# Performance work log

Hardware: AMD Instinct MI355X
Metric: run time of the kernel (lower is better)

## Reference

```python
import jax, jax.numpy as jnp
import numpy as np

EPS = 1e-7
TRUNC = 0.5          # truncation level of the robust L1 objective
K_CAND = 64          # max number of piecewise-linear extrema evaluated per row


def _pad_inf(v):
    # (B, n) -> (B, n+2) with -inf / +inf sentinels (torch _pad_inf)
    b = v.shape[0]
    return jnp.concatenate(
        [jnp.full((b, 1), -jnp.inf, v.dtype), v, jnp.full((b, 1), jnp.inf, v.dtype)], axis=-1)


def _pad_cumsum(c):
    # (B, n) -> (B, n+2): leading zero, trailing repeat of last (torch _pad_cumsum)
    return jnp.concatenate([jnp.zeros_like(c[:, :1]), c, c[:, -1:]], axis=-1)


_search_l = jax.vmap(lambda a, v: jnp.searchsorted(a, v, side='left'))
_search_r = jax.vmap(lambda a, v: jnp.searchsorted(a, v, side='right'))


def _align_trunc(x, y, w):
    # Solves min_a sum_i min(TRUNC, w_i * |a*x_i - y_i|) per row. x,y,w: (B, n).
    sign = jnp.sign(x)
    x = x * sign
    y = y * sign
    wx = w * x
    wy = w * y
    ydx = y / jnp.maximum(x, EPS)                       # breakpoints of |a x - y|
    cand_b = (wy - TRUNC) / jnp.maximum(wx, EPS)        # breakpoints where residual hits trunc
    cand_c = (wy + TRUNC) / jnp.maximum(wx, EPS)

    def sorted_cum(v):
        order = jnp.argsort(v, axis=-1)
        vs = jnp.take_along_axis(v, order, axis=-1)
        q = jnp.cumsum(jnp.take_along_axis(wx, order, axis=-1), axis=-1)
        return _pad_inf(vs), _pad_cumsum(q)

    As, QA = sorted_cum(ydx)
    Bs, QB = sorted_cum(cand_b)
    Cs, QC = sorted_cum(cand_c)

    def deriv(search):
        jA = search(As, ydx) - 1
        jB = search(Bs, ydx) - 1
        jC = search(Cs, ydx) - 1
        return (2 * jnp.take_along_axis(QA, jA, axis=-1)
                - jnp.take_along_axis(QB, jB, axis=-1)
                - jnp.take_along_axis(QC, jC, axis=-1))

    left_d = deriv(_search_l)
    right_d = deriv(_search_r)
    is_ext = (left_d < 0) & (right_d >= 0)
    is_ext = is_ext.at[:, 0].set(is_ext[:, 0] | ~jnp.any(is_ext, axis=-1))

    # first K_CAND extrema indices per row (stable sort: extrema=False-key first)
    cand_idx = jnp.argsort(~is_ext, axis=-1, stable=True)[:, :K_CAND]   # (B, K)
    valid = jnp.take_along_axis(is_ext, cand_idx, axis=-1)
    cand_a = jnp.take_along_axis(ydx, cand_idx, axis=-1)                # (B, K)

    # truncated-L1 residual at each candidate a: (B, K)
    res = jnp.sum(
        jnp.minimum(jnp.abs(cand_a[:, :, None] * x[:, None, :] - y[:, None, :]) * w[:, None, :], TRUNC),
        axis=-1)
    res = jnp.where(valid, res, jnp.inf)

    kbest = jnp.argmin(res, axis=-1)                                    # scatter_min equivalent
    loss = jnp.take_along_axis(res, kbest[:, None], axis=-1)[:, 0]
    index = jnp.take_along_axis(cand_idx, kbest[:, None], axis=-1)[:, 0]
    a = (jnp.take_along_axis(y, index[:, None], axis=-1)[:, 0]
         / jnp.maximum(jnp.take_along_axis(x, index[:, None], axis=-1)[:, 0], EPS))
    return a, loss, index


def setup_inputs() -> dict:
    key = jax.random.key(0)
    k1, k2, k3 = jax.random.split(key, 3)
    B, N = 256, 2048
    points_src = jax.random.normal(k1, (B, N, 3), dtype=jnp.float32)
    points_tgt = jax.random.normal(k2, (B, N, 3), dtype=jnp.float32)
    weight = jax.random.uniform(k3, (B, N), dtype=jnp.float32)  # weights >= 0
    return {"points_src": points_src, "points_tgt": points_tgt, "weight": weight}


def reference(points_src, points_tgt, weight):
    # align_points_scale: flatten (..., N, 3) -> (..., 3N), weight broadcast over xyz
    B = points_src.shape[0]
    x = points_src.reshape(B, -1)
    y = points_tgt.reshape(B, -1)
    w = jnp.broadcast_to(weight[..., None], points_src.shape).reshape(B, -1)
    a, loss, index = _align_trunc(x, y, w)
    return a
```

## Files before the change

kernel.cpp:

```cpp
#include <hip/hip_runtime.h>
#include <math.h>

#define NELEM   6144
#define NWEIGHT 2048
#define SORTN   8192
#define NT      1024
#define NWAVE   (NT / 64)
#define KCAND   64
#define DN      6146
#define PERT    (NELEM / NT)
#define CHUNK   (NELEM / NWAVE)

#define WINW     5.2e-3f
#define DELTARES 1.5e-3
#define WCAP     384

__device__ __forceinline__ int lb_idx(const float* __restrict__ key, float v) {
    int pos = 0;
#pragma unroll
    for (int step = SORTN >> 1; step > 0; step >>= 1)
        if (key[pos + step - 1] < v) pos += step;
    return pos;
}

#define CEK(a, b, up) { float lo = fminf(K[a], K[b]), hi = fmaxf(K[a], K[b]); \
                        K[a] = (up) ? lo : hi; K[b] = (up) ? hi : lo; }

__global__ __launch_bounds__(NT, 4)
void pointloss_align_kernel(const float* __restrict__ X,
                            const float* __restrict__ Y,
                            const float* __restrict__ W,
                            float* __restrict__ out)
{
    __shared__ __align__(16) unsigned char s_mem[155680];
    float*  s_ydx = (float*) (s_mem);
    float*  s_key = (float*) (s_mem + 24576);
    double* s_dlt = (double*)(s_mem + 57344);
    double* s_dle = (double*)(s_mem + 106512);
    double* s_wz   = (double*)(s_mem + 24576);
    double* s_wy2  = (double*)(s_mem + 73728);
    double* s_res  = (double*)(s_mem + 122880);
    int*    s_wind = (int*)   (s_mem + 123392);
    double* s_wres = (double*)(s_mem + 124928);

    __shared__ double s_wtot[2 * NWAVE];
    __shared__ double s_woff[2 * NWAVE];
    __shared__ int    s_isum[NWAVE];
    __shared__ int    s_cand[KCAND];
    __shared__ int    s_count;
    __shared__ int    s_fb;
    __shared__ float  s_wa;
    __shared__ int    s_wcnt;

    const int tid = threadIdx.x;
    const int row = blockIdx.x;
    const float* xb = X + (size_t)row * NELEM;
    const float* yb = Y + (size_t)row * NELEM;
    const float* wb = W + (size_t)row * NWEIGHT;

    float K[8];
    if (tid < NELEM / 8) {
        const int e0 = tid * 8;
        float4 x0 = *(const float4*)(xb + e0);
        float4 x1 = *(const float4*)(xb + e0 + 4);
        float4 y0 = *(const float4*)(yb + e0);
        float4 y1 = *(const float4*)(yb + e0 + 4);
        float xx[8] = {x0.x, x0.y, x0.z, x0.w, x1.x, x1.y, x1.z, x1.w};
        float yy[8] = {y0.x, y0.y, y0.z, y0.w, y1.x, y1.y, y1.z, y1.w};
#pragma unroll
        for (int r = 0; r < 8; ++r) {
            float x = xx[r], y = yy[r];
            float s = (x > 0.f) ? 1.f : ((x < 0.f) ? -1.f : 0.f);
            float z = x * s, y2 = y * s;
            K[r] = y2 / fmaxf(z, 1e-7f);
        }
        float4 o0 = {K[0], K[1], K[2], K[3]}, o1 = {K[4], K[5], K[6], K[7]};
        *(float4*)&s_ydx[e0]     = o0;
        *(float4*)&s_ydx[e0 + 4] = o1;
    } else {
#pragma unroll
        for (int r = 0; r < 8; ++r) K[r] = INFINITY;
    }
    for (int i = tid; i < DN; i += NT) { s_dlt[i] = 0.0; s_dle[i] = 0.0; }
    if (tid == 0) s_fb = 0;

    CEK(0, 1, true); CEK(2, 3, false); CEK(4, 5, true); CEK(6, 7, false);
    CEK(0, 2, true); CEK(1, 3, true);  CEK(4, 6, false); CEK(5, 7, false);
    CEK(0, 1, true); CEK(2, 3, true);  CEK(4, 5, false); CEK(6, 7, false);
    for (int kk = 8; kk <= 512; kk <<= 1) {
        const bool up = ((tid & (kk >> 3)) == 0);
        for (int jj = kk >> 1; jj >= 8; jj >>= 1) {
            const int m = jj >> 3;
            const bool tmin = (up == ((tid & m) == 0));
#pragma unroll
            for (int r = 0; r < 8; ++r) {
                float o = __shfl_xor(K[r], m);
                K[r] = tmin ? fminf(K[r], o) : fmaxf(K[r], o);
            }
        }
        CEK(0, 4, up); CEK(1, 5, up); CEK(2, 6, up); CEK(3, 7, up);
        CEK(0, 2, up); CEK(1, 3, up); CEK(4, 6, up); CEK(5, 7, up);
        CEK(0, 1, up); CEK(2, 3, up); CEK(4, 5, up); CEK(6, 7, up);
    }
    const int xv = ((tid >> 2) & 7) << 2;
    for (int kk = 1024; kk <= SORTN; kk <<= 1) {
        {
            float4 h0 = {K[0], K[1], K[2], K[3]}, h1 = {K[4], K[5], K[6], K[7]};
            *(float4*)&s_key[(8 * tid) ^ xv]       = h0;
            *(float4*)&s_key[(8 * tid + 4) ^ xv]   = h1;
        }
        __syncthreads();
        for (int jj = kk >> 1; jj >= 512; jj >>= 1) {
            for (int p = tid; p < SORTN / 2; p += NT) {
                const int i  = ((p & ~(jj - 1)) << 1) | (p & (jj - 1));
                const int ia = i ^ (((i >> 5) & 7) << 2);
                const int ib = ia ^ jj;
                const bool up = ((i & kk) == 0);
                float a = s_key[ia], b = s_key[ib];
                float lo = fminf(a, b), hi = fmaxf(a, b);
                s_key[ia] = up ? lo : hi;
                s_key[ib] = up ? hi : lo;
            }
            __syncthreads();
        }
        {
            float4 h0 = *(float4*)&s_key[(8 * tid) ^ xv];
            float4 h1 = *(float4*)&s_key[(8 * tid + 4) ^ xv];
            K[0] = h0.x; K[1] = h0.y; K[2] = h0.z; K[3] = h0.w;
            K[4] = h1.x; K[5] = h1.y; K[6] = h1.z; K[7] = h1.w;
        }
        __syncthreads();
        const bool up = ((tid & (kk >> 3)) == 0);
        for (int jj = 256; jj >= 8; jj >>= 1) {
            const int m = jj >> 3;
            const bool tmin = (up == ((tid & m) == 0));
#pragma unroll
            for (int r = 0; r < 8; ++r) {
                float o = __shfl_xor(K[r], m);
                K[r] = tmin ? fminf(K[r], o) : fmaxf(K[r], o);
            }
        }
        CEK(0, 4, up); CEK(1, 5, up); CEK(2, 6, up); CEK(3, 7, up);
        CEK(0, 2, up); CEK(1, 3, up); CEK(4, 6, up); CEK(5, 7, up);
        CEK(0, 1, up); CEK(2, 3, up); CEK(4, 5, up); CEK(6, 7, up);
    }
    {
        float4 h0 = {K[0], K[1], K[2], K[3]}, h1 = {K[4], K[5], K[6], K[7]};
        *(float4*)&s_key[8 * tid]     = h0;
        *(float4*)&s_key[8 * tid + 4] = h1;
    }
    __syncthreads();

    int lvq[PERT];
    {
        const int base = tid * PERT;
#pragma unroll
        for (int q = 0; q < PERT; ++q) {
            const int j = base + q;
            float x = xb[j], y = yb[j], w = wb[j / 3];
            float s = (x > 0.f) ? 1.f : ((x < 0.f) ? -1.f : 0.f);
            float z = x * s, y2 = y * s;
            float wx = w * z, wy = w * y2;
            float mwx = fmaxf(wx, 1e-7f);
            float bbv = (wy - 0.5f) / mwx;
            float ccv = (wy + 0.5f) / mwx;
            float v = s_ydx[j];
            int lv = lb_idx(s_key, v);
            int uv = lv; while (s_key[uv] == v) ++uv;
            int lbp = lb_idx(s_key, bbv);
            int ubp = lbp; while (s_key[ubp] == bbv) ++ubp;
            int lcp = lb_idx(s_key, ccv);
            int ucp = lcp; while (s_key[ucp] == ccv) ++ucp;
            lvq[q] = lv;
            double dwx = (double)wx;
            atomicAdd(&s_dlt[uv],  2.0 * dwx);
            atomicAdd(&s_dle[lv],  2.0 * dwx);
            atomicAdd(&s_dlt[ubp], -dwx);
            atomicAdd(&s_dle[lbp], -dwx);
            atomicAdd(&s_dlt[ucp], -dwx);
            atomicAdd(&s_dle[lcp], -dwx);
        }
    }
    __syncthreads();

    {
        const int lane = tid & 63, wv = tid >> 6;
        const int cbase = wv * CHUNK;
        double cl = 0.0, ce = 0.0;
#pragma unroll
        for (int k = 0; k < CHUNK / 64; ++k) {
            const int p = cbase + k * 64 + lane;
            double a = s_dlt[p], b = s_dle[p];
            for (int d = 1; d < 64; d <<= 1) {
                double ua = __shfl_up(a, d);
                double ub = __shfl_up(b, d);
                if (lane >= d) { a += ua; b += ub; }
            }
            a += cl; b += ce;
            s_dlt[p] = a; s_dle[p] = b;
            cl = __shfl(a, 63); ce = __shfl(b, 63);
        }
        if (lane == 63) { s_wtot[wv] = cl; s_wtot[NWAVE + wv] = ce; }
    }
    __syncthreads();
    if (tid < NWAVE) {
        double a = s_wtot[tid], b = s_wtot[NWAVE + tid];
        const double a0 = a, b0 = b;
        for (int d = 1; d < NWAVE; d <<= 1) {
            double ua = __shfl_up(a, d);
            double ub = __shfl_up(b, d);
            if (tid >= d) { a += ua; b += ub; }
        }
        s_woff[tid] = a - a0;
        s_woff[NWAVE + tid] = b - b0;
    }
    __syncthreads();

    {
        const int base = tid * PERT;
        unsigned char fl[PERT];
        int cnt = 0;
#pragma unroll
        for (int q = 0; q < PERT; ++q) {
            const int p = lvq[q];
            const int pw = p / CHUNK;
            double L = s_dlt[p] + s_woff[pw];
            double R = s_dle[p] + s_woff[NWAVE + pw];
            bool f = (L < 0.0) && (R >= 0.0);
            fl[q] = f ? 1 : 0; cnt += fl[q];
        }
        const int lane = tid & 63, wv = tid >> 6;
        int ti = cnt;
        for (int d = 1; d < 64; d <<= 1) {
            int u = __shfl_up(ti, d);
            if (lane >= d) ti += u;
        }
        if (lane == 63) s_isum[wv] = ti;
        __syncthreads();
        int off = 0;
        for (int q = 0; q < wv; ++q) off += s_isum[q];
        const int ex = off + ti - cnt;
        if (tid == NT - 1) s_count = ex + cnt;
        int pos = ex;
#pragma unroll
        for (int q = 0; q < PERT; ++q) {
            if (fl[q]) { if (pos < KCAND) s_cand[pos] = base + q; ++pos; }
        }
    }
    __syncthreads();
    if (tid == 0 && s_count == 0) { s_cand[0] = 0; s_count = 1; s_fb = 1; }
    __syncthreads();

    for (int e = tid; e < NELEM; e += NT) {
        double x = (double)xb[e], y = (double)yb[e], w = (double)wb[e / 3];
        double s = (x > 0.0) ? 1.0 : ((x < 0.0) ? -1.0 : 0.0);
        s_wz[e]  = w * (x * s);
        s_wy2[e] = w * (y * s);
    }
    __syncthreads();

    {
        const int lane = tid & 63, wv = tid >> 6;
        const int count = s_count;
        double acc[4] = {0.0, 0.0, 0.0, 0.0};
        double ak[4];
#pragma unroll
        for (int q = 0; q < 4; ++q) {
            int c = 4 * wv + q;
            ak[q] = (c < count) ? (double)s_ydx[s_cand[c]] : 0.0;
        }
        for (int e = lane; e < NELEM; e += 64) {
            double a = s_wz[e], b = s_wy2[e];
#pragma unroll
            for (int q = 0; q < 4; ++q)
                acc[q] += fmin(fabs(fma(ak[q], a, -b)), 0.5);
        }
#pragma unroll
        for (int q = 0; q < 4; ++q)
            for (int d = 32; d > 0; d >>= 1) acc[q] += __shfl_xor(acc[q], d);
        if (lane == 0) {
#pragma unroll
            for (int q = 0; q < 4; ++q) {
                int c = 4 * wv + q;
                s_res[c] = (c < count) ? acc[q] : (double)INFINITY;
            }
        }
    }
    __syncthreads();
    if (tid < KCAND) {
        double rv = s_res[tid];
        int kb = tid;
        for (int d = 32; d > 0; d >>= 1) {
            double ro = __shfl_xor(rv, d);
            int   ko = __shfl_xor(kb, d);
            if (ro < rv || (ro == rv && ko < kb)) { rv = ro; kb = ko; }
        }
        if (tid == 0) s_wa = s_ydx[s_cand[kb]];
    }
    __syncthreads();

    const float awin = s_wa;
    if (tid == 0) s_wcnt = 0;
    __syncthreads();
    if (!s_fb) {
        for (int j = tid; j < NELEM; j += NT) {
            if (fabsf(s_ydx[j] - awin) <= WINW) {
                int p = atomicAdd(&s_wcnt, 1);
                if (p < WCAP) s_wind[p] = j;
            }
        }
    }
    __syncthreads();
    const int wtot = s_wcnt;
    const int wcnt = (wtot < WCAP) ? wtot : WCAP;
    const bool commit = (s_fb != 0) || (wtot > WCAP);
    const int rounds = commit ? 0 : ((wcnt + 63) >> 6);

    {
        const int lane = tid & 63, wv = tid >> 6;
        for (int rd = 0; rd < rounds; ++rd) {
            const int cb = rd << 6;
            if (cb + 4 * wv >= wcnt) continue;
            double acc[4] = {0.0, 0.0, 0.0, 0.0};
            double ak[4];
#pragma unroll
            for (int q = 0; q < 4; ++q) {
                int idx = cb + 4 * wv + q;
                ak[q] = (idx < wcnt) ? (double)s_ydx[s_wind[idx]] : 0.0;
            }
            for (int e = lane; e < NELEM; e += 64) {
                double a = s_wz[e], b = s_wy2[e];
#pragma unroll
                for (int q = 0; q < 4; ++q)
                    acc[q] += fmin(fabs(fma(ak[q], a, -b)), 0.5);
            }
#pragma unroll
            for (int q = 0; q < 4; ++q)
                for (int d = 32; d > 0; d >>= 1) acc[q] += __shfl_xor(acc[q], d);
            if (lane == 0) {
#pragma unroll
                for (int q = 0; q < 4; ++q) {
                    int idx = cb + 4 * wv + q;
                    if (idx < wcnt) s_wres[idx] = acc[q];
                }
            }
        }
    }
    __syncthreads();

    if (tid == 0) {
        float outv = awin;
        if (!commit && wcnt > 0) {
            double rmin = INFINITY;
            for (int i = 0; i < wcnt; ++i) rmin = fmin(rmin, s_wres[i]);
            double A = INFINITY, B = -INFINITY;
            for (int i = 0; i < wcnt; ++i) {
                double excess = s_wres[i] - rmin;
                if (excess <= DELTARES) {
                    double a = (double)s_ydx[s_wind[i]];
                    A = fmin(A, a + excess);
                    B = fmax(B, a - excess);
                }
            }
            outv = (float)(0.5 * (A + B));
        }
        out[row] = outv;
    }
}

extern "C" void kernel_launch(void* const* d_in, const int* in_sizes, int n_in,
                              void* d_out, int out_size, void* d_ws, size_t ws_size,
                              hipStream_t stream) {
    const float* X = (const float*)d_in[0];
    const float* Y = (const float*)d_in[1];
    const float* W = (const float*)d_in[2];
    float* out = (float*)d_out;
    const int nrows = in_sizes[0] / NELEM;
    pointloss_align_kernel<<<dim3(nrows), dim3(NT), 0, stream>>>(X, Y, W, out);
}
```

Measured before the change: 120.0 us.

## Switch derivative and residual math to int/float and shrink shared memory

Replaces the double-precision derivative accumulation with fixed-point int atomics scaled by 32768. Residual evaluation now runs in float with one candidate per wave instead of four per wave in double. The stored ydx array is dropped and recomputed from global x and y where needed, and the binary search is bounded to 6144 elements. Together these cut LDS from about 155KB to about 74KB, and launch bounds are raised to allow more occupancy. The cost is precision: weights are quantised in the derivative sums and residuals are float sums over 6144 terms, which can change which candidate wins against a 1.5e-3 tolerance.

```diff
diff --git a/kernel.cpp b/kernel.cpp
--- a/kernel.cpp
+++ b/kernel.cpp
@@ -10,47 +10,50 @@
 #define DN      6146
 #define PERT    (NELEM / NT)
 #define CHUNK   (NELEM / NWAVE)
+#define QSCALE  32768.0f
 
 #define WINW     5.2e-3f
 #define DELTARES 1.5e-3
 #define WCAP     384
 
-__device__ __forceinline__ int lb_idx(const float* __restrict__ key, float v) {
+__device__ __forceinline__ int lb6144(const float* __restrict__ key, float v) {
     int pos = 0;
 #pragma unroll
-    for (int step = SORTN >> 1; step > 0; step >>= 1)
-        if (key[pos + step - 1] < v) pos += step;
+    for (int step = 4096; step > 0; step >>= 1) {
+        int np = pos + step;
+        if (np <= NELEM && key[np - 1] < v) pos = np;
+    }
     return pos;
 }
 
 #define CEK(a, b, up) { float lo = fminf(K[a], K[b]), hi = fmaxf(K[a], K[b]); \
                         K[a] = (up) ? lo : hi; K[b] = (up) ? hi : lo; }
 
-__global__ __launch_bounds__(NT, 4)
+__global__ __launch_bounds__(NT, 8)
 void pointloss_align_kernel(const float* __restrict__ X,
                             const float* __restrict__ Y,
                             const float* __restrict__ W,
                             float* __restrict__ out)
 {
-    __shared__ __align__(16) unsigned char s_mem[155680];
-    float*  s_ydx = (float*) (s_mem);
-    float*  s_key = (float*) (s_mem + 24576);
-    double* s_dlt = (double*)(s_mem + 57344);
-    double* s_dle = (double*)(s_mem + 106512);
-    double* s_wz   = (double*)(s_mem + 24576);
-    double* s_wy2  = (double*)(s_mem + 73728);
-    double* s_res  = (double*)(s_mem + 122880);
-    int*    s_wind = (int*)   (s_mem + 123392);
-    double* s_wres = (double*)(s_mem + 124928);
-
-    __shared__ double s_wtot[2 * NWAVE];
-    __shared__ double s_woff[2 * NWAVE];
-    __shared__ int    s_isum[NWAVE];
-    __shared__ int    s_cand[KCAND];
-    __shared__ int    s_count;
-    __shared__ int    s_fb;
-    __shared__ float  s_wa;
-    __shared__ int    s_wcnt;
+    __shared__ __align__(16) unsigned char s_mem[73744];
+    float* s_sort = (float*)s_mem;
+    float* s_key  = (float*)s_mem;
+    int*   s_dlt  = (int*)  (s_mem + 24576);
+    int*   s_dle  = (int*)  (s_mem + 49160);
+    float* s_wzf  = (float*)(s_mem + 24576);
+    float* s_wy2  = (float*)(s_mem + 49160);
+
+    __shared__ int   s_wtot[2 * NWAVE];
+    __shared__ int   s_woff[2 * NWAVE];
+    __shared__ int   s_isum[NWAVE];
+    __shared__ int   s_cand[KCAND];
+    __shared__ float s_res[KCAND];
+    __shared__ int   s_wind[WCAP];
+    __shared__ float s_wres[WCAP];
+    __shared__ int   s_count;
+    __shared__ int   s_fb;
+    __shared__ float s_wa;
+    __shared__ int   s_wcnt;
 
     const int tid = threadIdx.x;
     const int row = blockIdx.x;
@@ -71,17 +74,12 @@
         for (int r = 0; r < 8; ++r) {
             float x = xx[r], y = yy[r];
             float s = (x > 0.f) ? 1.f : ((x < 0.f) ? -1.f : 0.f);
-            float z = x * s, y2 = y * s;
-            K[r] = y2 / fmaxf(z, 1e-7f);
-        }
-        float4 o0 = {K[0], K[1], K[2], K[3]}, o1 = {K[4], K[5], K[6], K[7]};
-        *(float4*)&s_ydx[e0]     = o0;
-        *(float4*)&s_ydx[e0 + 4] = o1;
+            K[r] = (y * s) / fmaxf(x * s, 1e-7f);
+        }
     } else {
 #pragma unroll
         for (int r = 0; r < 8; ++r) K[r] = INFINITY;
     }
-    for (int i = tid; i < DN; i += NT) { s_dlt[i] = 0.0; s_dle[i] = 0.0; }
     if (tid == 0) s_fb = 0;
 
     CEK(0, 1, true); CEK(2, 3, false); CEK(4, 5, true); CEK(6, 7, false);
@@ -106,8 +104,8 @@
     for (int kk = 1024; kk <= SORTN; kk <<= 1) {
         {
             float4 h0 = {K[0], K[1], K[2], K[3]}, h1 = {K[4], K[5], K[6], K[7]};
-            *(float4*)&s_key[(8 * tid) ^ xv]       = h0;
-            *(float4*)&s_key[(8 * tid + 4) ^ xv]   = h1;
+            *(float4*)&s_sort[(8 * tid) ^ xv]     = h0;
+            *(float4*)&s_sort[(8 * tid + 4) ^ xv] = h1;
         }
         __syncthreads();
         for (int jj = kk >> 1; jj >= 512; jj >>= 1) {
@@ -116,16 +114,16 @@
                 const int ia = i ^ (((i >> 5) & 7) << 2);
                 const int ib = ia ^ jj;
                 const bool up = ((i & kk) == 0);
-                float a = s_key[ia], b = s_key[ib];
+                float a = s_sort[ia], b = s_sort[ib];
                 float lo = fminf(a, b), hi = fmaxf(a, b);
-                s_key[ia] = up ? lo : hi;
-                s_key[ib] = up ? hi : lo;
+                s_sort[ia] = up ? lo : hi;
+                s_sort[ib] = up ? hi : lo;
             }
             __syncthreads();
         }
         {
-            float4 h0 = *(float4*)&s_key[(8 * tid) ^ xv];
-            float4 h1 = *(float4*)&s_key[(8 * tid + 4) ^ xv];
+            float4 h0 = *(float4*)&s_sort[(8 * tid) ^ xv];
+            float4 h1 = *(float4*)&s_sort[(8 * tid + 4) ^ xv];
             K[0] = h0.x; K[1] = h0.y; K[2] = h0.z; K[3] = h0.w;
             K[4] = h1.x; K[5] = h1.y; K[6] = h1.z; K[7] = h1.w;
         }
@@ -144,11 +142,12 @@
         CEK(0, 2, up); CEK(1, 3, up); CEK(4, 6, up); CEK(5, 7, up);
         CEK(0, 1, up); CEK(2, 3, up); CEK(4, 5, up); CEK(6, 7, up);
     }
-    {
+    if (tid < NELEM / 8) {
         float4 h0 = {K[0], K[1], K[2], K[3]}, h1 = {K[4], K[5], K[6], K[7]};
         *(float4*)&s_key[8 * tid]     = h0;
         *(float4*)&s_key[8 * tid + 4] = h1;
     }
+    for (int i = tid; i < DN; i += NT) { s_dlt[i] = 0; s_dle[i] = 0; }
     __syncthreads();
 
     int lvq[PERT];
@@ -164,21 +163,21 @@
             float mwx = fmaxf(wx, 1e-7f);
             float bbv = (wy - 0.5f) / mwx;
             float ccv = (wy + 0.5f) / mwx;
-            float v = s_ydx[j];
-            int lv = lb_idx(s_key, v);
-            int uv = lv; while (s_key[uv] == v) ++uv;
-            int lbp = lb_idx(s_key, bbv);
-            int ubp = lbp; while (s_key[ubp] == bbv) ++ubp;
-            int lcp = lb_idx(s_key, ccv);
-            int ucp = lcp; while (s_key[ucp] == ccv) ++ucp;
+            float v = y2 / fmaxf(z, 1e-7f);
+            int lv = lb6144(s_key, v);
+            int uv = lv; while (uv < NELEM && s_key[uv] == v) ++uv;
+            int lbp = lb6144(s_key, bbv);
+            int ubp = lbp; while (ubp < NELEM && s_key[ubp] == bbv) ++ubp;
+            int lcp = lb6144(s_key, ccv);
+            int ucp = lcp; while (ucp < NELEM && s_key[ucp] == ccv) ++ucp;
             lvq[q] = lv;
-            double dwx = (double)wx;
-            atomicAdd(&s_dlt[uv],  2.0 * dwx);
-            atomicAdd(&s_dle[lv],  2.0 * dwx);
-            atomicAdd(&s_dlt[ubp], -dwx);
-            atomicAdd(&s_dle[lbp], -dwx);
-            atomicAdd(&s_dlt[ucp], -dwx);
-            atomicAdd(&s_dle[lcp], -dwx);
+            int qx = __float2int_rn(wx * QSCALE);
+            atomicAdd(&s_dlt[uv],  2 * qx);
+            atomicAdd(&s_dle[lv],  2 * qx);
+            atomicAdd(&s_dlt[ubp], -qx);
+            atomicAdd(&s_dle[lbp], -qx);
+            atomicAdd(&s_dlt[ucp], -qx);
+            atomicAdd(&s_dle[lcp], -qx);
         }
     }
     __syncthreads();
@@ -186,14 +185,14 @@
     {
         const int lane = tid & 63, wv = tid >> 6;
         const int cbase = wv * CHUNK;
-        double cl = 0.0, ce = 0.0;
+        int cl = 0, ce = 0;
 #pragma unroll
         for (int k = 0; k < CHUNK / 64; ++k) {
             const int p = cbase + k * 64 + lane;
-            double a = s_dlt[p], b = s_dle[p];
+            int a = s_dlt[p], b = s_dle[p];
             for (int d = 1; d < 64; d <<= 1) {
-                double ua = __shfl_up(a, d);
-                double ub = __shfl_up(b, d);
+                int ua = __shfl_up(a, d);
+                int ub = __shfl_up(b, d);
                 if (lane >= d) { a += ua; b += ub; }
             }
             a += cl; b += ce;
@@ -204,11 +203,11 @@
     }
     __syncthreads();
     if (tid < NWAVE) {
-        double a = s_wtot[tid], b = s_wtot[NWAVE + tid];
-        const double a0 = a, b0 = b;
+        int a = s_wtot[tid], b = s_wtot[NWAVE + tid];
+        const int a0 = a, b0 = b;
         for (int d = 1; d < NWAVE; d <<= 1) {
-            double ua = __shfl_up(a, d);
-            double ub = __shfl_up(b, d);
+            int ua = __shfl_up(a, d);
+            int ub = __shfl_up(b, d);
             if (tid >= d) { a += ua; b += ub; }
         }
         s_woff[tid] = a - a0;
@@ -224,9 +223,9 @@
         for (int q = 0; q < PERT; ++q) {
             const int p = lvq[q];
             const int pw = p / CHUNK;
-            double L = s_dlt[p] + s_woff[pw];
-            double R = s_dle[p] + s_woff[NWAVE + pw];
-            bool f = (L < 0.0) && (R >= 0.0);
+            int L = s_dlt[p] + s_woff[pw];
+            int R = s_dle[p] + s_woff[NWAVE + pw];
+            bool f = (L < 0) && (R >= 0);
             fl[q] = f ? 1 : 0; cnt += fl[q];
         }
         const int lane = tid & 63, wv = tid >> 6;
@@ -252,59 +251,55 @@
     __syncthreads();
 
     for (int e = tid; e < NELEM; e += NT) {
-        double x = (double)xb[e], y = (double)yb[e], w = (double)wb[e / 3];
-        double s = (x > 0.0) ? 1.0 : ((x < 0.0) ? -1.0 : 0.0);
-        s_wz[e]  = w * (x * s);
+        float x = xb[e], y = yb[e], w = wb[e / 3];
+        float s = (x > 0.f) ? 1.f : ((x < 0.f) ? -1.f : 0.f);
+        s_wzf[e] = w * (x * s);
         s_wy2[e] = w * (y * s);
     }
     __syncthreads();
 
+    const int lane = tid & 63, wv = tid >> 6;
     {
-        const int lane = tid & 63, wv = tid >> 6;
-        const int count = s_count;
-        double acc[4] = {0.0, 0.0, 0.0, 0.0};
-        double ak[4];
-#pragma unroll
-        for (int q = 0; q < 4; ++q) {
-            int c = 4 * wv + q;
-            ak[q] = (c < count) ? (double)s_ydx[s_cand[c]] : 0.0;
-        }
-        for (int e = lane; e < NELEM; e += 64) {
-            double a = s_wz[e], b = s_wy2[e];
-#pragma unroll
-            for (int q = 0; q < 4; ++q)
-                acc[q] += fmin(fabs(fma(ak[q], a, -b)), 0.5);
-        }
-#pragma unroll
-        for (int q = 0; q < 4; ++q)
-            for (int d = 32; d > 0; d >>= 1) acc[q] += __shfl_xor(acc[q], d);
-        if (lane == 0) {
-#pragma unroll
-            for (int q = 0; q < 4; ++q) {
-                int c = 4 * wv + q;
-                s_res[c] = (c < count) ? acc[q] : (double)INFINITY;
-            }
-        }
-    }
+        const int cnt64 = (s_count < KCAND) ? s_count : KCAND;
+        for (int c = wv; c < cnt64; c += NWAVE) {
+            const int j = s_cand[c];
+            float x = xb[j], y = yb[j];
+            float s = (x > 0.f) ? 1.f : ((x < 0.f) ? -1.f : 0.f);
+            float ak = (y * s) / fmaxf(x * s, 1e-7f);
+            float acc = 0.f;
+            for (int e = lane; e < NELEM; e += 64)
+                acc += fminf(fabsf(fmaf(ak, s_wzf[e], -s_wy2[e])), 0.5f);
+            for (int d = 32; d > 0; d >>= 1) acc += __shfl_xor(acc, d);
+            if (lane == 0) s_res[c] = acc;
+        }
+    }
+    if (tid == 0) s_wcnt = 0;
     __syncthreads();
     if (tid < KCAND) {
-        double rv = s_res[tid];
+        const int cnt64 = (s_count < KCAND) ? s_count : KCAND;
+        float rv = (tid < cnt64) ? s_res[tid] : INFINITY;
         int kb = tid;
         for (int d = 32; d > 0; d >>= 1) {
-            double ro = __shfl_xor(rv, d);
+            float ro = __shfl_xor(rv, d);
             int   ko = __shfl_xor(kb, d);
             if (ro < rv || (ro == rv && ko < kb)) { rv = ro; kb = ko; }
         }
-        if (tid == 0) s_wa = s_ydx[s_cand[kb]];
+        if (tid == 0) {
+            const int j = s_cand[kb];
+            float x = xb[j], y = yb[j];
+            float s = (x > 0.f) ? 1.f : ((x < 0.f) ? -1.f : 0.f);
+            s_wa = (y * s) / fmaxf(x * s, 1e-7f);
+        }
     }
     __syncthreads();
 
     const float awin = s_wa;
-    if (tid == 0) s_wcnt = 0;
-    __syncthreads();
     if (!s_fb) {
         for (int j = tid; j < NELEM; j += NT) {
-            if (fabsf(s_ydx[j] - awin) <= WINW) {
+            float x = xb[j], y = yb[j];
+            float s = (x > 0.f) ? 1.f : ((x < 0.f) ? -1.f : 0.f);
+            float v = (y * s) / fmaxf(x * s, 1e-7f);
+            if (fabsf(v - awin) <= WINW) {
                 int p = atomicAdd(&s_wcnt, 1);
                 if (p < WCAP) s_wind[p] = j;
             }
@@ -314,36 +309,17 @@
     const int wtot = s_wcnt;
     const int wcnt = (wtot < WCAP) ? wtot : WCAP;
     const bool commit = (s_fb != 0) || (wtot > WCAP);
-    const int rounds = commit ? 0 : ((wcnt + 63) >> 6);
-
-    {
-        const int lane = tid & 63, wv = tid >> 6;
-        for (int rd = 0; rd < rounds; ++rd) {
-            const int cb = rd << 6;
-            if (cb + 4 * wv >= wcnt) continue;
-            double acc[4] = {0.0, 0.0, 0.0, 0.0};
-            double ak[4];
-#pragma unroll
-            for (int q = 0; q < 4; ++q) {
-                int idx = cb + 4 * wv + q;
-                ak[q] = (idx < wcnt) ? (double)s_ydx[s_wind[idx]] : 0.0;
-            }
-            for (int e = lane; e < NELEM; e += 64) {
-                double a = s_wz[e], b = s_wy2[e];
-#pragma unroll
-                for (int q = 0; q < 4; ++q)
-                    acc[q] += fmin(fabs(fma(ak[q], a, -b)), 0.5);
-            }
-#pragma unroll
-            for (int q = 0; q < 4; ++q)
-                for (int d = 32; d > 0; d >>= 1) acc[q] += __shfl_xor(acc[q], d);
-            if (lane == 0) {
-#pragma unroll
-                for (int q = 0; q < 4; ++q) {
-                    int idx = cb + 4 * wv + q;
-                    if (idx < wcnt) s_wres[idx] = acc[q];
-                }
-            }
+    if (!commit) {
+        for (int c = wv; c < wcnt; c += NWAVE) {
+            const int j = s_wind[c];
+            float x = xb[j], y = yb[j];
+            float s = (x > 0.f) ? 1.f : ((x < 0.f) ? -1.f : 0.f);
+            float ak = (y * s) / fmaxf(x * s, 1e-7f);
+            float acc = 0.f;
+            for (int e = lane; e < NELEM; e += 64)
+                acc += fminf(fabsf(fmaf(ak, s_wzf[e], -s_wy2[e])), 0.5f);
+            for (int d = 32; d > 0; d >>= 1) acc += __shfl_xor(acc, d);
+            if (lane == 0) s_wres[c] = acc;
         }
     }
     __syncthreads();
@@ -352,12 +328,15 @@
         float outv = awin;
         if (!commit && wcnt > 0) {
             double rmin = INFINITY;
-            for (int i = 0; i < wcnt; ++i) rmin = fmin(rmin, s_wres[i]);
+            for (int i = 0; i < wcnt; ++i) rmin = fmin(rmin, (double)s_wres[i]);
             double A = INFINITY, B = -INFINITY;
             for (int i = 0; i < wcnt; ++i) {
-                double excess = s_wres[i] - rmin;
+                double excess = (double)s_wres[i] - rmin;
                 if (excess <= DELTARES) {
-                    double a = (double)s_ydx[s_wind[i]];
+                    const int j = s_wind[i];
+                    float x = xb[j], y = yb[j];
+                    float s = (x > 0.f) ? 1.f : ((x < 0.f) ? -1.f : 0.f);
+                    double a = (double)((y * s) / fmaxf(x * s, 1e-7f));
                     A = fmin(A, a + excess);
                     B = fmax(B, a - excess);
                 }
```

New measurement: 107.5 us. 1.12x faster.
